# Kernel optimization log

Measured on AMD Instinct MI355X. Metric: run time of the kernel, lower is better.

The kernel has to match this reference:

```python
import jax, jax.numpy as jnp
import numpy as np
import math

D_MODEL = 512
NHEAD = 8
N_LAYERS = 3
D_FF = 2048
INPUT_DIM = 128
NUM_CLASSES = 64
FACTOR = 5


def setup_inputs() -> dict:
    key = jax.random.key(0)
    ks = jax.random.split(key, 24)
    s = 0.02
    d, f, nl = D_MODEL, D_FF, N_LAYERS
    inp = {
        "x": jax.random.normal(ks[0], (4, 1024, INPUT_DIM), dtype=jnp.float32),
        "W_emb": jax.random.normal(ks[1], (INPUT_DIM, d), dtype=jnp.float32) * s,
        "b_emb": jnp.zeros((d,), jnp.float32),
        "Wq": jax.random.normal(ks[2], (nl, d, d), dtype=jnp.float32) * s,
        "bq": jnp.zeros((nl, d), jnp.float32),
        "Wk": jax.random.normal(ks[3], (nl, d, d), dtype=jnp.float32) * s,
        "bk": jnp.zeros((nl, d), jnp.float32),
        "Wv": jax.random.normal(ks[4], (nl, d, d), dtype=jnp.float32) * s,
        "bv": jnp.zeros((nl, d), jnp.float32),
        "Wo": jax.random.normal(ks[5], (nl, d, d), dtype=jnp.float32) * s,
        "bo": jnp.zeros((nl, d), jnp.float32),
        "ln1_g": jnp.ones((nl, d), jnp.float32),
        "ln1_b": jnp.zeros((nl, d), jnp.float32),
        "W1": jax.random.normal(ks[6], (nl, d, f), dtype=jnp.float32) * s,
        "b1": jnp.zeros((nl, f), jnp.float32),
        "W2": jax.random.normal(ks[7], (nl, f, d), dtype=jnp.float32) * s,
        "b2": jnp.zeros((nl, d), jnp.float32),
        "ln2_g": jnp.ones((nl, d), jnp.float32),
        "ln2_b": jnp.zeros((nl, d), jnp.float32),
        "W_dec": jax.random.normal(ks[8], (d, NUM_CLASSES), dtype=jnp.float32) * s,
        "b_dec": jnp.zeros((NUM_CLASSES,), jnp.float32),
    }
    return inp


def _layer_norm(x, g, b, eps=1e-5):
    m = jnp.mean(x, axis=-1, keepdims=True)
    v = jnp.var(x, axis=-1, keepdims=True)
    return (x - m) * jax.lax.rsqrt(v + eps) * g + b


def _pos_encoding(L, d):
    pos = jnp.arange(L, dtype=jnp.float32)[:, None]
    div = jnp.exp(jnp.arange(0, d, 2, dtype=jnp.float32) * (-math.log(10000.0) / d))
    pe = jnp.zeros((L, d), jnp.float32)
    pe = pe.at[:, 0::2].set(jnp.sin(pos * div))
    pe = pe.at[:, 1::2].set(jnp.cos(pos * div))
    return pe


def _prob_sparse_attn(x, Wq, bq, Wk, bk, Wv, bv, Wo, bo):
    B, L, d = x.shape
    H, dk = NHEAD, d // NHEAD
    u = min(L, int(FACTOR * math.log(L)) if L > 1 else L)
    Q = (x @ Wq + bq).reshape(B, L, H, dk).transpose(0, 2, 1, 3)  # bhld
    K = (x @ Wk + bk).reshape(B, L, H, dk).transpose(0, 2, 1, 3)
    V = (x @ Wv + bv).reshape(B, L, H, dk).transpose(0, 2, 1, 3)
    scores = jnp.einsum("bhld,bhmd->bhlm", Q, K) / math.sqrt(dk)  # [B,H,L,L]
    kth = jax.lax.top_k(scores, u)[0][..., -1:]  # kth-largest per row
    scores = jnp.where(scores < kth, -10000.0, scores)
    attn = jax.nn.softmax(scores, axis=-1)
    out = jnp.einsum("bhlm,bhmd->bhld", attn, V)
    out = out.transpose(0, 2, 1, 3).reshape(B, L, d)
    return out @ Wo + bo


def reference(x, W_emb, b_emb, Wq, bq, Wk, bk, Wv, bv, Wo, bo,
              ln1_g, ln1_b, W1, b1, W2, b2, ln2_g, ln2_b, W_dec, b_dec):
    B, L, _ = x.shape
    h = (x @ W_emb + b_emb) * math.sqrt(D_MODEL)
    h = h + _pos_encoding(L, D_MODEL)[None]
    for i in range(N_LAYERS):
        a = _prob_sparse_attn(h, Wq[i], bq[i], Wk[i], bk[i], Wv[i], bv[i], Wo[i], bo[i])
        h = _layer_norm(h + a, ln1_g[i], ln1_b[i])
        ff = jax.nn.relu(h @ W1[i] + b1[i]) @ W2[i] + b2[i]
        h = _layer_norm(h + ff, ln2_g[i], ln2_b[i])
    return h @ W_dec + b_dec
```

## Files before the change

kernel.cpp:

```cpp
#include <hip/hip_runtime.h>
#include <math.h>

#define SEQ 1024
#define BATCH 4
#define DMODEL 512
#define NHEAD 8
#define DK 64
#define DFF 2048
#define U_TOP 34
#define ROWS (BATCH * SEQ)

typedef unsigned short ushort_t;
typedef __attribute__((ext_vector_type(8))) short short8;
typedef __attribute__((ext_vector_type(4))) float float4v;

__device__ inline ushort_t f2bf(float f) {
  unsigned u = __float_as_uint(f);
  unsigned r = u + 0x7fffu + ((u >> 16) & 1u);
  return (ushort_t)(r >> 16);
}
__device__ inline float bf2f(ushort_t u) {
  return __uint_as_float((unsigned)u << 16);
}
__device__ inline float keyinv(unsigned cand) {
  unsigned fb = (cand & 0x80000000u) ? (cand ^ 0x80000000u) : ~cand;
  return __uint_as_float(fb);
}

__device__ inline void glds16(const void* g, void* l) {
  __builtin_amdgcn_global_load_lds(
      (const __attribute__((address_space(1))) unsigned int*)g,
      (__attribute__((address_space(3))) unsigned int*)l, 16, 0, 0);
}

template <int RELU, int OUTBF16, int EPI, int ADDC>
__global__ __launch_bounds__(256) void gemm64(
    const ushort_t* __restrict__ A, const short* __restrict__ Bt,
    const float* __restrict__ b0, const float* __restrict__ b1,
    const float* __restrict__ b2, void* __restrict__ Cout,
    const ushort_t* __restrict__ Cadd, int K, int N, int zWstride,
    int zCstride) {
  __shared__ short As[64 * 32];
  __shared__ short Bs[64 * 32];

  const int tid = threadIdx.x;
  const int lane = tid & 63, w = tid >> 6;
  const int wm = w >> 1, wn = w & 1;
  const int quad = lane >> 4, r16 = lane & 15;
  const int bm = blockIdx.y * 64, bn = blockIdx.x * 64;
  const int z = blockIdx.z;
  const short* Bz = Bt + (size_t)z * zWstride;
  const float* bias = (z == 0) ? b0 : (z == 1 ? b1 : b2);

  const int srow = tid >> 2, skseg = tid & 3;
  const ushort_t* Ag = A + (size_t)(bm + srow) * K + skseg * 8;
  const short* Bg = Bz + (size_t)(bn + srow) * K + skseg * 8;
  short* lA = As + w * 512;
  short* lB = Bs + w * 512;

  float4v acc[2][2];
#pragma unroll
  for (int m = 0; m < 2; ++m)
#pragma unroll
    for (int n = 0; n < 2; ++n) acc[m][n] = (float4v){0.f, 0.f, 0.f, 0.f};

  for (int k0 = 0; k0 < K; k0 += 32) {
    __syncthreads();
    glds16(Ag + k0, lA);
    glds16(Bg + k0, lB);
    __syncthreads();

    short8 af[2], bfr[2];
#pragma unroll
    for (int m = 0; m < 2; ++m)
      af[m] = *(const short8*)&As[(wm * 32 + m * 16 + r16) * 32 + quad * 8];
#pragma unroll
    for (int n = 0; n < 2; ++n)
      bfr[n] = *(const short8*)&Bs[(wn * 32 + n * 16 + r16) * 32 + quad * 8];
#pragma unroll
    for (int m = 0; m < 2; ++m)
#pragma unroll
      for (int n = 0; n < 2; ++n)
        acc[m][n] = __builtin_amdgcn_mfma_f32_16x16x32_bf16(af[m], bfr[n],
                                                            acc[m][n], 0, 0, 0);
  }

  const float pe_c = (float)(-9.210340371976184 / 512.0);
  const float sqrtd = 22.62741699796952f;

  float bias_n[2];
#pragma unroll
  for (int n = 0; n < 2; ++n) bias_n[n] = bias[bn + wn * 32 + n * 16 + r16];

#pragma unroll
  for (int m = 0; m < 2; ++m) {
#pragma unroll
    for (int n = 0; n < 2; ++n) {
      int col = bn + wn * 32 + n * 16 + r16;
#pragma unroll
      for (int reg = 0; reg < 4; ++reg) {
        int row = bm + wm * 32 + m * 16 + quad * 4 + reg;
        float v = acc[m][n][reg] + bias_n[n];
        if (RELU) v = fmaxf(v, 0.f);
        if (EPI == 2) {
          int pos = row & (SEQ - 1);
          float e = __expf((float)(col & ~1) * pe_c);
          float arg = (float)pos * e;
          v = v * sqrtd + ((col & 1) ? __cosf(arg) : __sinf(arg));
        }
        if (ADDC) v += bf2f(Cadd[(size_t)row * N + col]);
        if (OUTBF16) {
          ushort_t* C = (ushort_t*)Cout + (size_t)z * zCstride;
          C[(size_t)row * N + col] = f2bf(v);
        } else {
          float* C = (float*)Cout + (size_t)z * zCstride;
          C[(size_t)row * N + col] = v;
        }
      }
    }
  }
}

__global__ __launch_bounds__(256) void convert_all(
    const float* __restrict__ Wq, const float* __restrict__ Wk,
    const float* __restrict__ Wv, const float* __restrict__ Wo,
    const float* __restrict__ W1, const float* __restrict__ W2,
    const float* __restrict__ W_emb, const float* __restrict__ W_dec,
    short* __restrict__ wt) {
  __shared__ float t[32][33];
  int id = blockIdx.x;
  const float* src;
  short* dst;
  int K, N, tk, tn;
  if (id < 9216) {
    int lay = id / 3072, r = id % 3072;
    short* wl = wt + (size_t)lay * 3145728;
    const size_t wsz = 512 * 512;
    if (r < 1024) {
      int wi = r >> 8, tile = r & 255;
      const float* base = (wi == 0) ? Wq : (wi == 1) ? Wk : (wi == 2) ? Wv : Wo;
      src = base + lay * wsz;
      dst = wl + wi * 262144;
      K = 512; N = 512; tk = tile >> 4; tn = tile & 15;
    } else if (r < 2048) {
      int tile = r - 1024;
      src = W1 + (size_t)lay * 512 * 2048;
      dst = wl + 1048576;
      K = 512; N = 2048; tk = tile >> 6; tn = tile & 63;
    } else {
      int tile = r - 2048;
      src = W2 + (size_t)lay * 2048 * 512;
      dst = wl + 2097152;
      K = 2048; N = 512; tk = tile >> 4; tn = tile & 15;
    }
  } else {
    int r = id - 9216;
    if (r < 64) {
      src = W_emb; dst = wt + 9437184; K = 128; N = 512; tk = r >> 4; tn = r & 15;
    } else {
      r -= 64;
      src = W_dec; dst = wt + 9502720; K = 512; N = 64; tk = r >> 1; tn = r & 1;
    }
  }
  const int k0 = tk * 32, n0 = tn * 32;
  const int tx = threadIdx.x, ty = threadIdx.y;
#pragma unroll
  for (int i = 0; i < 4; ++i) {
    int r = ty + i * 8;
    t[r][tx] = src[(size_t)(k0 + r) * N + n0 + tx];
  }
  __syncthreads();
#pragma unroll
  for (int i = 0; i < 4; ++i) {
    int r = ty + i * 8;
    dst[(size_t)(n0 + r) * K + k0 + tx] = (short)f2bf(t[tx][r]);
  }
}

__global__ __launch_bounds__(256) void f32_to_bf16_kernel(
    const float* __restrict__ src, ushort_t* __restrict__ dst) {
  int i = blockIdx.x * blockDim.x + threadIdx.x;
  float4 v = ((const float4*)src)[i];
  ushort4 o;
  o.x = f2bf(v.x); o.y = f2bf(v.y); o.z = f2bf(v.z); o.w = f2bf(v.w);
  ((ushort4*)dst)[i] = o;
}

__global__ __launch_bounds__(256) void ln_kernel(
    const ushort_t* __restrict__ t1b, const float* __restrict__ g,
    const float* __restrict__ bb, ushort_t* __restrict__ hb) {
  const int row = blockIdx.x * 4 + (threadIdx.x >> 6);
  const int lane = threadIdx.x & 63;
  const size_t base = (size_t)row * DMODEL + lane * 8;
  uint4 raw = *(const uint4*)(t1b + base);
  unsigned rr[4] = {raw.x, raw.y, raw.z, raw.w};
  float v[8];
#pragma unroll
  for (int k = 0; k < 4; ++k) {
    v[2 * k] = bf2f((ushort_t)(rr[k] & 0xffff));
    v[2 * k + 1] = bf2f((ushort_t)(rr[k] >> 16));
  }
  float sum = 0.f, sq = 0.f;
#pragma unroll
  for (int k = 0; k < 8; ++k) { sum += v[k]; sq += v[k] * v[k]; }
#pragma unroll
  for (int off = 32; off; off >>= 1) {
    sum += __shfl_xor(sum, off);
    sq += __shfl_xor(sq, off);
  }
  float mean = sum * (1.f / 512.f);
  float var = fmaxf(sq * (1.f / 512.f) - mean * mean, 0.f);
  float rstd = 1.f / sqrtf(var + 1e-5f);
  float4 g0 = *(const float4*)(g + lane * 8);
  float4 g1 = *(const float4*)(g + lane * 8 + 4);
  float4 c0 = *(const float4*)(bb + lane * 8);
  float4 c1 = *(const float4*)(bb + lane * 8 + 4);
  float gg[8] = {g0.x, g0.y, g0.z, g0.w, g1.x, g1.y, g1.z, g1.w};
  float cc[8] = {c0.x, c0.y, c0.z, c0.w, c1.x, c1.y, c1.z, c1.w};
  uint4 out;
  unsigned* op = (unsigned*)&out;
#pragma unroll
  for (int k = 0; k < 4; ++k) {
    float y0 = (v[2 * k] - mean) * rstd * gg[2 * k] + cc[2 * k];
    float y1 = (v[2 * k + 1] - mean) * rstd * gg[2 * k + 1] + cc[2 * k + 1];
    op[k] = (unsigned)f2bf(y0) | ((unsigned)f2bf(y1) << 16);
  }
  *(uint4*)(hb + base) = out;
}

#define SSTR 1028

__global__ __launch_bounds__(1024, 8) void attn_kernel(
    const ushort_t* __restrict__ Qb, const ushort_t* __restrict__ Kb,
    const ushort_t* __restrict__ Vb, ushort_t* __restrict__ Ob) {
  __shared__ float s[16 * SSTR];
  __shared__ int jlist[16][64];
  __shared__ float wlist[16][64];

  const int tid = threadIdx.x;
  const int q0 = blockIdx.x * 16;
  const int h = blockIdx.y;
  const int b = blockIdx.z;
  const int w = tid >> 6;
  const int lane = tid & 63;
  const int quad = lane >> 4, r16 = lane & 15;

  {
    const int j0 = w * 64;
    const ushort_t* qrow =
        Qb + (size_t)(b * SEQ + q0 + r16) * DMODEL + h * DK + quad * 8;
    short8 aq0 = *(const short8*)qrow;
    short8 aq1 = *(const short8*)(qrow + 32);

    float4v acc[4];
#pragma unroll
    for (int nt = 0; nt < 4; ++nt) {
      const ushort_t* krow =
          Kb + (size_t)(b * SEQ + j0 + nt * 16 + r16) * DMODEL + h * DK +
          quad * 8;
      short8 bk0 = *(const short8*)krow;
      short8 bk1 = *(const short8*)(krow + 32);
      float4v a = (float4v){0.f, 0.f, 0.f, 0.f};
      a = __builtin_amdgcn_mfma_f32_16x16x32_bf16(aq0, bk0, a, 0, 0, 0);
      a = __builtin_amdgcn_mfma_f32_16x16x32_bf16(aq1, bk1, a, 0, 0, 0);
      acc[nt] = a;
    }
#pragma unroll
    for (int nt = 0; nt < 4; ++nt)
#pragma unroll
      for (int reg = 0; reg < 4; ++reg)
        s[(quad * 4 + reg) * SSTR + j0 + nt * 16 + r16] =
            acc[nt][reg] * 0.125f;
  }
  __syncthreads();

  {
    float v[16];
    float lmax = -1e30f;
#pragma unroll
    for (int i = 0; i < 16; ++i) {
      float f = s[w * SSTR + lane + 64 * i];
      v[i] = f;
      lmax = fmaxf(lmax, f);
    }
    float mx = lmax;
#pragma unroll
    for (int off = 32; off; off >>= 1) mx = fmaxf(mx, __shfl_xor(mx, off));

    unsigned ansT = 0u;
    {
      bool ex = false;
      for (int bit = 31; bit >= 0 && !ex; --bit) {
        unsigned cand = ansT | (1u << bit);
        float fc = keyinv(cand);
        int c = (int)__popcll(__ballot(lmax >= fc));
        if (c >= U_TOP) { ansT = cand; ex = (c == U_TOP); }
      }
    }
    const float fT = keyinv(ansT);

    int total = 0;
#pragma unroll
    for (int i = 0; i < 16; ++i)
      total += (int)__popcll(__ballot(v[i] >= fT));

    const unsigned long long lmask_lt = (1ull << lane) - 1ull;
    float* tmpv = &wlist[w][0];
    int* tmpj = &jlist[w][0];
    int ncand;
    if (total <= 64) {
      int basec = 0;
#pragma unroll
      for (int i = 0; i < 16; ++i) {
        bool gk = v[i] >= fT;
        unsigned long long mask = __ballot(gk);
        if (gk) {
          int p = basec + (int)__popcll(mask & lmask_lt);
          tmpv[p] = v[i];
          tmpj[p] = lane + 64 * i;
        }
        basec += (int)__popcll(mask);
      }
      ncand = basec;
    } else {
      unsigned ans = 0u;
      int cge = 1024, bit = 31;
      bool ex = false;
      while (bit >= 0 && cge > 64 && !ex) {
        unsigned cand = ans | (1u << bit);
        float fc = keyinv(cand);
        int c = 0;
#pragma unroll
        for (int i = 0; i < 16; ++i) c += (int)__popcll(__ballot(v[i] >= fc));
        if (c >= U_TOP) { ans = cand; cge = c; ex = (c == U_TOP); }
        --bit;
      }
      float fa = keyinv(ans);
      int basec = 0;
#pragma unroll
      for (int i = 0; i < 16; ++i) {
        bool gk = v[i] >= fa;
        unsigned long long mask = __ballot(gk);
        if (gk) {
          int p = basec + (int)__popcll(mask & lmask_lt);
          if (p < 64) { tmpv[p] = v[i]; tmpj[p] = lane + 64 * i; }
        }
        basec += (int)__popcll(mask);
      }
      ncand = basec > 64 ? 64 : basec;
    }

    float cf = (lane < ncand) ? tmpv[lane] : -3.4e38f;
    int cj = (lane < ncand) ? tmpj[lane] : 0;

    unsigned ansB = 0u;
    {
      bool ex = false;
      for (int bit = 31; bit >= 0 && !ex; --bit) {
        unsigned cand = ansB | (1u << bit);
        float fc = keyinv(cand);
        int c = (int)__popcll(__ballot(cf >= fc));
        if (c >= U_TOP) { ansB = cand; ex = (c == U_TOP); }
      }
    }
    const float thr = keyinv(ansB);

    bool keep = cf >= thr;
    unsigned long long kmask = __ballot(keep);
    int n = (int)__popcll(kmask);
    float e = keep ? __expf(cf - mx) : 0.f;
    float zsum = e;
#pragma unroll
    for (int off = 32; off; off >>= 1) zsum += __shfl_xor(zsum, off);
    int pos = (int)__popcll(kmask & lmask_lt);
    if (keep) { jlist[w][pos] = cj; wlist[w][pos] = e; }

    const ushort_t* vbase = Vb + (size_t)b * SEQ * DMODEL + h * DK;
    float o = 0.f;
    int i = 0;
    for (; i + 4 <= n; i += 4) {
      int j0 = jlist[w][i], j1 = jlist[w][i + 1];
      int j2 = jlist[w][i + 2], j3 = jlist[w][i + 3];
      float w0 = wlist[w][i], w1 = wlist[w][i + 1];
      float w2 = wlist[w][i + 2], w3 = wlist[w][i + 3];
      float p0 = bf2f(vbase[(size_t)j0 * DMODEL + lane]);
      float p1 = bf2f(vbase[(size_t)j1 * DMODEL + lane]);
      float p2 = bf2f(vbase[(size_t)j2 * DMODEL + lane]);
      float p3 = bf2f(vbase[(size_t)j3 * DMODEL + lane]);
      o += w0 * p0 + w1 * p1 + w2 * p2 + w3 * p3;
    }
    for (; i < n; ++i)
      o += wlist[w][i] * bf2f(vbase[(size_t)jlist[w][i] * DMODEL + lane]);
    o /= zsum;
    Ob[(size_t)(b * SEQ + q0 + w) * DMODEL + h * DK + lane] = f2bf(o);
  }
}

extern "C" void kernel_launch(void* const* d_in, const int* in_sizes, int n_in,
                              void* d_out, int out_size, void* d_ws,
                              size_t ws_size, hipStream_t stream) {
  const float* x = (const float*)d_in[0];
  const float* W_emb = (const float*)d_in[1];
  const float* b_emb = (const float*)d_in[2];
  const float* Wq = (const float*)d_in[3];
  const float* bq = (const float*)d_in[4];
  const float* Wk = (const float*)d_in[5];
  const float* bk = (const float*)d_in[6];
  const float* Wv = (const float*)d_in[7];
  const float* bv = (const float*)d_in[8];
  const float* Wo = (const float*)d_in[9];
  const float* bo = (const float*)d_in[10];
  const float* ln1_g = (const float*)d_in[11];
  const float* ln1_b = (const float*)d_in[12];
  const float* W1 = (const float*)d_in[13];
  const float* b1 = (const float*)d_in[14];
  const float* W2 = (const float*)d_in[15];
  const float* b2 = (const float*)d_in[16];
  const float* ln2_g = (const float*)d_in[17];
  const float* ln2_b = (const float*)d_in[18];
  const float* W_dec = (const float*)d_in[19];
  const float* b_dec = (const float*)d_in[20];

  char* wsb = (char*)d_ws;
  ushort_t* qkv = (ushort_t*)wsb;
  ushort_t* ffh = (ushort_t*)wsb;
  ushort_t* ao = (ushort_t*)(wsb + ((size_t)16 << 20));
  ushort_t* xb = (ushort_t*)(wsb + ((size_t)16 << 20));
  ushort_t* t1b = (ushort_t*)(wsb + ((size_t)20 << 20));
  ushort_t* hb = (ushort_t*)(wsb + ((size_t)24 << 20));
  short* wt = (short*)(wsb + ((size_t)28 << 20));
  short* wembT = wt + 9437184;
  short* wdecT = wt + 9502720;

  f32_to_bf16_kernel<<<dim3(512), 256, 0, stream>>>(x, xb);
  convert_all<<<dim3(9312), dim3(32, 8), 0, stream>>>(Wq, Wk, Wv, Wo, W1, W2,
                                                      W_emb, W_dec, wt);
  gemm64<0, 1, 2, 0><<<dim3(8, 64), 256, 0, stream>>>(
      xb, wembT, b_emb, b_emb, b_emb, (void*)hb, nullptr, 128, 512, 0, 0);

  for (int i = 0; i < 3; ++i) {
    short* wtL = wt + (size_t)i * 3145728;

    gemm64<0, 1, 0, 0><<<dim3(8, 64, 3), 256, 0, stream>>>(
        hb, wtL, bq + i * DMODEL, bk + i * DMODEL, bv + i * DMODEL,
        (void*)qkv, nullptr, 512, 512, 262144, 2097152);

    attn_kernel<<<dim3(SEQ / 16, NHEAD, BATCH), dim3(1024), 0, stream>>>(
        qkv, qkv + 2097152, qkv + 4194304, ao);

    gemm64<0, 1, 0, 1><<<dim3(8, 64), 256, 0, stream>>>(
        ao, wtL + 786432, bo + i * DMODEL, bo + i * DMODEL, bo + i * DMODEL,
        (void*)t1b, hb, 512, 512, 0, 0);
    ln_kernel<<<dim3(ROWS / 4), 256, 0, stream>>>(
        t1b, ln1_g + i * DMODEL, ln1_b + i * DMODEL, hb);

    gemm64<1, 1, 0, 0><<<dim3(32, 64), 256, 0, stream>>>(
        hb, wtL + 1048576, b1 + i * DFF, b1 + i * DFF, b1 + i * DFF,
        (void*)ffh, nullptr, 512, 2048, 0, 0);
    gemm64<0, 1, 0, 1><<<dim3(8, 64), 256, 0, stream>>>(
        ffh, wtL + 2097152, b2 + i * DMODEL, b2 + i * DMODEL, b2 + i * DMODEL,
        (void*)t1b, hb, 2048, 512, 0, 0);
    ln_kernel<<<dim3(ROWS / 4), 256, 0, stream>>>(
        t1b, ln2_g + i * DMODEL, ln2_b + i * DMODEL, hb);
  }

  gemm64<0, 0, 0, 0><<<dim3(1, 64), 256, 0, stream>>>(
      hb, wdecT, b_dec, b_dec, b_dec, d_out, nullptr, 512, 64, 0, 0);
}
```

Before: 575.1 us.

## Add 128x128-tile GEMM for QKV and FFN1, streamline top-k candidate gather

Adds a gemm128 kernel in which each of the four waves computes a 64x64 sub-tile with 4x4 MFMA accumulators. It is used for the fused QKV projection, treated as a single N=1536 GEMM that splits its output into Q/K/V by column, and for the FFN up-projection, to raise operand reuse and cut redundant global loads. The attention top-k path now does one ballot-compaction pass directly and only refines the threshold when more than 64 candidates exist, which removes the separate counting pass. The cost is higher register pressure and fewer blocks for the larger tiles (384 and 512 blocks).

Result: no change. 578.9 us (+0.7%).

```diff
diff --git a/kernel.cpp b/kernel.cpp
--- a/kernel.cpp
+++ b/kernel.cpp
@@ -33,13 +33,92 @@
       (__attribute__((address_space(3))) unsigned int*)l, 16, 0, 0);
 }
 
+template <int RELU, int SPLIT>
+__global__ __launch_bounds__(256) void gemm128(
+    const ushort_t* __restrict__ A, const short* __restrict__ Bt,
+    const float* __restrict__ b0, const float* __restrict__ b1,
+    const float* __restrict__ b2, ushort_t* __restrict__ Cout,
+    int K, int N, int zCstride) {
+  __shared__ short As[128 * 32];
+  __shared__ short Bs[128 * 32];
+
+  const int tid = threadIdx.x;
+  const int lane = tid & 63, w = tid >> 6;
+  const int wm = w >> 1, wn = w & 1;
+  const int quad = lane >> 4, r16 = lane & 15;
+  const int bm = blockIdx.y * 128, bn = blockIdx.x * 128;
+
+  const int srow = lane >> 2, skseg = lane & 3;
+  const ushort_t* Ag0 = A + (size_t)(bm + w * 16 + srow) * K + skseg * 8;
+  const ushort_t* Ag1 = Ag0 + (size_t)64 * K;
+  const short* Bg0 = Bt + (size_t)(bn + w * 16 + srow) * K + skseg * 8;
+  const short* Bg1 = Bg0 + (size_t)64 * K;
+  short* lA0 = As + (w * 16) * 32;
+  short* lA1 = As + (64 + w * 16) * 32;
+  short* lB0 = Bs + (w * 16) * 32;
+  short* lB1 = Bs + (64 + w * 16) * 32;
+
+  float4v acc[4][4];
+#pragma unroll
+  for (int m = 0; m < 4; ++m)
+#pragma unroll
+    for (int n = 0; n < 4; ++n) acc[m][n] = (float4v){0.f, 0.f, 0.f, 0.f};
+
+  for (int k0 = 0; k0 < K; k0 += 32) {
+    __syncthreads();
+    glds16(Ag0 + k0, lA0);
+    glds16(Ag1 + k0, lA1);
+    glds16(Bg0 + k0, lB0);
+    glds16(Bg1 + k0, lB1);
+    __syncthreads();
+
+    short8 af[4], bfr[4];
+#pragma unroll
+    for (int m = 0; m < 4; ++m)
+      af[m] = *(const short8*)&As[(wm * 64 + m * 16 + r16) * 32 + quad * 8];
+#pragma unroll
+    for (int n = 0; n < 4; ++n)
+      bfr[n] = *(const short8*)&Bs[(wn * 64 + n * 16 + r16) * 32 + quad * 8];
+#pragma unroll
+    for (int m = 0; m < 4; ++m)
+#pragma unroll
+      for (int n = 0; n < 4; ++n)
+        acc[m][n] = __builtin_amdgcn_mfma_f32_16x16x32_bf16(af[m], bfr[n],
+                                                            acc[m][n], 0, 0, 0);
+  }
+
+  const int z = SPLIT ? (bn >> 9) : 0;
+  const float* bias = (z == 0) ? b0 : (z == 1 ? b1 : b2);
+  const int cbase = SPLIT ? (bn & 511) : bn;
+  const int strideN = SPLIT ? 512 : N;
+  ushort_t* C = Cout + (SPLIT ? (size_t)z * zCstride : (size_t)0);
+
+  float bias_n[4];
+#pragma unroll
+  for (int n = 0; n < 4; ++n)
+    bias_n[n] = bias[cbase + wn * 64 + n * 16 + r16];
+
+#pragma unroll
+  for (int m = 0; m < 4; ++m) {
+#pragma unroll
+    for (int n = 0; n < 4; ++n) {
+      int col = cbase + wn * 64 + n * 16 + r16;
+#pragma unroll
+      for (int reg = 0; reg < 4; ++reg) {
+        int row = bm + wm * 64 + m * 16 + quad * 4 + reg;
+        float v = acc[m][n][reg] + bias_n[n];
+        if (RELU) v = fmaxf(v, 0.f);
+        C[(size_t)row * strideN + col] = f2bf(v);
+      }
+    }
+  }
+}
+
 template <int RELU, int OUTBF16, int EPI, int ADDC>
 __global__ __launch_bounds__(256) void gemm64(
     const ushort_t* __restrict__ A, const short* __restrict__ Bt,
-    const float* __restrict__ b0, const float* __restrict__ b1,
-    const float* __restrict__ b2, void* __restrict__ Cout,
-    const ushort_t* __restrict__ Cadd, int K, int N, int zWstride,
-    int zCstride) {
+    const float* __restrict__ bias, void* __restrict__ Cout,
+    const ushort_t* __restrict__ Cadd, int K, int N) {
   __shared__ short As[64 * 32];
   __shared__ short Bs[64 * 32];
 
@@ -48,13 +127,10 @@
   const int wm = w >> 1, wn = w & 1;
   const int quad = lane >> 4, r16 = lane & 15;
   const int bm = blockIdx.y * 64, bn = blockIdx.x * 64;
-  const int z = blockIdx.z;
-  const short* Bz = Bt + (size_t)z * zWstride;
-  const float* bias = (z == 0) ? b0 : (z == 1 ? b1 : b2);
 
   const int srow = tid >> 2, skseg = tid & 3;
   const ushort_t* Ag = A + (size_t)(bm + srow) * K + skseg * 8;
-  const short* Bg = Bz + (size_t)(bn + srow) * K + skseg * 8;
+  const short* Bg = Bt + (size_t)(bn + srow) * K + skseg * 8;
   short* lA = As + w * 512;
   short* lB = Bs + w * 512;
 
@@ -110,11 +186,9 @@
         }
         if (ADDC) v += bf2f(Cadd[(size_t)row * N + col]);
         if (OUTBF16) {
-          ushort_t* C = (ushort_t*)Cout + (size_t)z * zCstride;
-          C[(size_t)row * N + col] = f2bf(v);
+          ((ushort_t*)Cout)[(size_t)row * N + col] = f2bf(v);
         } else {
-          float* C = (float*)Cout + (size_t)z * zCstride;
-          C[(size_t)row * N + col] = v;
+          ((float*)Cout)[(size_t)row * N + col] = v;
         }
       }
     }
@@ -299,32 +373,25 @@
     }
     const float fT = keyinv(ansT);
 
-    int total = 0;
-#pragma unroll
-    for (int i = 0; i < 16; ++i)
-      total += (int)__popcll(__ballot(v[i] >= fT));
-
     const unsigned long long lmask_lt = (1ull << lane) - 1ull;
     float* tmpv = &wlist[w][0];
     int* tmpj = &jlist[w][0];
-    int ncand;
-    if (total <= 64) {
-      int basec = 0;
-#pragma unroll
-      for (int i = 0; i < 16; ++i) {
-        bool gk = v[i] >= fT;
-        unsigned long long mask = __ballot(gk);
-        if (gk) {
-          int p = basec + (int)__popcll(mask & lmask_lt);
-          tmpv[p] = v[i];
-          tmpj[p] = lane + 64 * i;
-        }
-        basec += (int)__popcll(mask);
-      }
-      ncand = basec;
-    } else {
-      unsigned ans = 0u;
-      int cge = 1024, bit = 31;
+
+    int basec = 0;
+#pragma unroll
+    for (int i = 0; i < 16; ++i) {
+      bool gk = v[i] >= fT;
+      unsigned long long mask = __ballot(gk);
+      if (gk) {
+        int p = basec + (int)__popcll(mask & lmask_lt);
+        if (p < 64) { tmpv[p] = v[i]; tmpj[p] = lane + 64 * i; }
+      }
+      basec += (int)__popcll(mask);
+    }
+    int ncand = basec;
+    if (basec > 64) {
+      unsigned ans = ansT;
+      int cge = basec, bit = 31;
       bool ex = false;
       while (bit >= 0 && cge > 64 && !ex) {
         unsigned cand = ans | (1u << bit);
@@ -336,18 +403,18 @@
         --bit;
       }
       float fa = keyinv(ans);
-      int basec = 0;
+      int b2 = 0;
 #pragma unroll
       for (int i = 0; i < 16; ++i) {
         bool gk = v[i] >= fa;
         unsigned long long mask = __ballot(gk);
         if (gk) {
-          int p = basec + (int)__popcll(mask & lmask_lt);
+          int p = b2 + (int)__popcll(mask & lmask_lt);
           if (p < 64) { tmpv[p] = v[i]; tmpj[p] = lane + 64 * i; }
         }
-        basec += (int)__popcll(mask);
-      }
-      ncand = basec > 64 ? 64 : basec;
+        b2 += (int)__popcll(mask);
+      }
+      ncand = b2 > 64 ? 64 : b2;
     }
 
     float cf = (lane < ncand) ? tmpv[lane] : -3.4e38f;
@@ -436,34 +503,31 @@
   convert_all<<<dim3(9312), dim3(32, 8), 0, stream>>>(Wq, Wk, Wv, Wo, W1, W2,
                                                       W_emb, W_dec, wt);
   gemm64<0, 1, 2, 0><<<dim3(8, 64), 256, 0, stream>>>(
-      xb, wembT, b_emb, b_emb, b_emb, (void*)hb, nullptr, 128, 512, 0, 0);
+      xb, wembT, b_emb, (void*)hb, nullptr, 128, 512);
 
   for (int i = 0; i < 3; ++i) {
     short* wtL = wt + (size_t)i * 3145728;
 
-    gemm64<0, 1, 0, 0><<<dim3(8, 64, 3), 256, 0, stream>>>(
-        hb, wtL, bq + i * DMODEL, bk + i * DMODEL, bv + i * DMODEL,
-        (void*)qkv, nullptr, 512, 512, 262144, 2097152);
+    gemm128<0, 1><<<dim3(12, 32), 256, 0, stream>>>(
+        hb, wtL, bq + i * DMODEL, bk + i * DMODEL, bv + i * DMODEL, qkv, 512,
+        512, 2097152);
 
     attn_kernel<<<dim3(SEQ / 16, NHEAD, BATCH), dim3(1024), 0, stream>>>(
         qkv, qkv + 2097152, qkv + 4194304, ao);
 
     gemm64<0, 1, 0, 1><<<dim3(8, 64), 256, 0, stream>>>(
-        ao, wtL + 786432, bo + i * DMODEL, bo + i * DMODEL, bo + i * DMODEL,
-        (void*)t1b, hb, 512, 512, 0, 0);
+        ao, wtL + 786432, bo + i * DMODEL, (void*)t1b, hb, 512, 512);
     ln_kernel<<<dim3(ROWS / 4), 256, 0, stream>>>(
         t1b, ln1_g + i * DMODEL, ln1_b + i * DMODEL, hb);
 
-    gemm64<1, 1, 0, 0><<<dim3(32, 64), 256, 0, stream>>>(
-        hb, wtL + 1048576, b1 + i * DFF, b1 + i * DFF, b1 + i * DFF,
-        (void*)ffh, nullptr, 512, 2048, 0, 0);
+    gemm128<1, 0><<<dim3(16, 32), 256, 0, stream>>>(
+        hb, wtL + 1048576, b1 + i * DFF, nullptr, nullptr, ffh, 512, 2048, 0);
     gemm64<0, 1, 0, 1><<<dim3(8, 64), 256, 0, stream>>>(
-        ffh, wtL + 2097152, b2 + i * DMODEL, b2 + i * DMODEL, b2 + i * DMODEL,
-        (void*)t1b, hb, 2048, 512, 0, 0);
+        ffh, wtL + 2097152, b2 + i * DMODEL, (void*)t1b, hb, 2048, 512);
     ln_kernel<<<dim3(ROWS / 4), 256, 0, stream>>>(
         t1b, ln2_g + i * DMODEL, ln2_b + i * DMODEL, hb);
   }
 
   gemm64<0, 0, 0, 0><<<dim3(1, 64), 256, 0, stream>>>(
-      hb, wdecT, b_dec, b_dec, b_dec, d_out, nullptr, 512, 64, 0, 0);
-}
+      hb, wdecT, b_dec, d_out, nullptr, 512, 64);
+}
```
